# Performance work log

Hardware: AMD Instinct MI355X
Metric: run time of the kernel (lower is better)

The kernel has to match this reference:

```python
import jax, jax.numpy as jnp
import numpy as np

# CrossAttention (DFFNet): 1x1 convs produce q,k from depth and v from rgb;
# full dense attention over hw spatial tokens: softmax(q^T k) then v @ mask^T.

def setup_inputs() -> dict:
    key = jax.random.key(0)
    ks = jax.random.split(key, 8)
    B, C, H, W = 4, 256, 64, 64
    Cqk = C // 8  # ratio=8 -> 32
    s = 0.02
    return {
        "rgb":   jax.random.normal(ks[0], (B, C, H, W), jnp.float32),
        "depth": jax.random.normal(ks[1], (B, C, H, W), jnp.float32),
        "Wq": jax.random.normal(ks[2], (Cqk, C), jnp.float32) * s,
        "bq": jax.random.normal(ks[3], (Cqk,), jnp.float32) * s,
        "Wk": jax.random.normal(ks[4], (Cqk, C), jnp.float32) * s,
        "bk": jax.random.normal(ks[5], (Cqk,), jnp.float32) * s,
        "Wv": jax.random.normal(ks[6], (C, C), jnp.float32) * s,
        "bv": jax.random.normal(ks[7], (C,), jnp.float32) * s,
    }


def reference(rgb, depth, Wq, bq, Wk, bk, Wv, bv):
    B, C, H, W = rgb.shape
    hw = H * W
    d = depth.reshape(B, C, hw)   # [B, C, hw]
    r = rgb.reshape(B, C, hw)     # [B, C, hw]
    # 1x1 convs == channel-mixing linear maps
    q = jnp.einsum('oc,bcn->bon', Wq, d) + bq[None, :, None]  # [B, Cqk, hw]
    k = jnp.einsum('oc,bcn->bon', Wk, d) + bk[None, :, None]  # [B, Cqk, hw]
    v = jnp.einsum('oc,bcn->bon', Wv, r) + bv[None, :, None]  # [B, C, hw]
    # scores: q^T k -> [B, hw, hw], softmax over last dim
    scores = jnp.einsum('bcn,bcm->bnm', q, k)
    mask = jax.nn.softmax(scores, axis=-1)
    # feat = v @ mask^T  -> [B, C, hw]
    feat = jnp.einsum('bcm,bnm->bcn', v, mask)
    return feat.reshape(B, C, H, W)
```

## Files before the change

### kernel.cpp

```cpp
#include <hip/hip_runtime.h>
#include <stdint.h>

#define L2E 1.44269504088896340736f

typedef _Float16 half8 __attribute__((ext_vector_type(8)));
typedef float floatx4 __attribute__((ext_vector_type(4)));

static __device__ __forceinline__ unsigned short f32_to_f16u(float f) {
  union { _Float16 h; unsigned short s; } cv; cv.h = (_Float16)f; return cv.s;
}

typedef __attribute__((address_space(3))) unsigned int as3_uint;
typedef __attribute__((address_space(1))) const unsigned int as1_cuint;

static __device__ __forceinline__ void async16(const void* g, void* l) {
  __builtin_amdgcn_global_load_lds((as1_cuint*)g, (as3_uint*)l, 16, 0, 0);
}

__global__ __launch_bounds__(256) void proj_kernel(
    const float* __restrict__ rgb,
    const float* __restrict__ depth,
    const float* __restrict__ Wq, const float* __restrict__ bq,
    const float* __restrict__ Wk, const float* __restrict__ bk,
    const float* __restrict__ Wv, const float* __restrict__ bv,
    unsigned short* __restrict__ qT,
    unsigned short* __restrict__ kT,
    unsigned short* __restrict__ v)
{
  __shared__ __align__(16) unsigned short sW[64 * 256];

  const int n0 = blockIdx.x * 64;
  const int b  = blockIdx.y;
  const int z  = blockIdx.z;
  const int t  = threadIdx.x;
  const int w  = t >> 6;
  const int lane = t & 63;
  const int l15 = lane & 15;
  const int q4  = lane >> 4;

  const float* X = (z == 0) ? depth : rgb;
  const float* xb = X + (size_t)b * 256 * 4096;
  const int n_row = n0 + 16 * w + l15;

  half8 a8[8];
#pragma unroll
  for (int ks = 0; ks < 8; ks++) {
#pragma unroll
    for (int j = 0; j < 8; j++) {
      int c = ks * 32 + q4 * 8 + j;
      a8[ks][j] = (_Float16)xb[(size_t)c * 4096 + n_row];
    }
  }

  const int nq = (z == 0) ? 1 : 2;
  for (int qd = 0; qd < nq; qd++) {
    const int colbase = (z == 0) ? 0 : (z - 1) * 128 + qd * 64;
    __syncthreads();

#pragma unroll
    for (int it = 0; it < 8; it++) {
      int L = it * 256 + t;
      int og = L >> 5;
      int phys = L & 31;
      int ci = phys ^ (og & 7);
      const float* wr;
      if (z == 0) wr = (og < 32) ? (Wq + (size_t)og * 256) : (Wk + (size_t)(og - 32) * 256);
      else        wr = Wv + (size_t)(colbase + og) * 256;
      float4 w0 = *(const float4*)(wr + ci * 8);
      float4 w1 = *(const float4*)(wr + ci * 8 + 4);
      half8 h;
      h[0] = (_Float16)w0.x; h[1] = (_Float16)w0.y; h[2] = (_Float16)w0.z; h[3] = (_Float16)w0.w;
      h[4] = (_Float16)w1.x; h[5] = (_Float16)w1.y; h[6] = (_Float16)w1.z; h[7] = (_Float16)w1.w;
      *(half8*)&sW[(size_t)L * 8] = h;
    }

    float bias[4];
#pragma unroll
    for (int ct = 0; ct < 4; ct++) {
      int og = ct * 16 + l15;
      if (z == 0) bias[ct] = (og < 32) ? bq[og] : bk[og - 32];
      else        bias[ct] = bv[colbase + og];
    }
    __syncthreads();

    floatx4 acc[4];
#pragma unroll
    for (int i = 0; i < 4; i++) acc[i] = (floatx4){0.f, 0.f, 0.f, 0.f};

#pragma unroll
    for (int ks = 0; ks < 8; ks++) {
      const int ci = ks * 4 + q4;
#pragma unroll
      for (int ct = 0; ct < 4; ct++) {
        int og = ct * 16 + l15;
        half8 bf = *(const half8*)&sW[og * 256 + ((ci ^ (og & 7)) * 8)];
        acc[ct] = __builtin_amdgcn_mfma_f32_16x16x32_f16(a8[ks], bf, acc[ct], 0, 0, 0);
      }
    }

    __syncthreads();

    if (z == 0) {
#pragma unroll
      for (int ct = 0; ct < 4; ct++) {
        int og = ct * 16 + l15;
#pragma unroll
        for (int r = 0; r < 4; r++) {
          int n = n0 + 16 * w + q4 * 4 + r;
          unsigned short hv = f32_to_f16u(acc[ct][r] + bias[ct]);
          if (og < 32) qT[((size_t)b * 4096 + n) * 32 + og] = hv;
          else         kT[((size_t)b * 4096 + n) * 32 + (og - 32)] = hv;
        }
      }
    } else {
      unsigned short* tile = sW;
#pragma unroll
      for (int ct = 0; ct < 4; ct++) {
#pragma unroll
        for (int r = 0; r < 4; r++) {
          int co_l = ct * 16 + l15;
          int nl = 16 * w + q4 * 4 + r;
          tile[co_l * 72 + nl] = f32_to_f16u(acc[ct][r] + bias[ct]);
        }
      }
      __syncthreads();
#pragma unroll
      for (int it = 0; it < 2; it++) {
        int co_l = it * 32 + (t >> 3);
        int ch = t & 7;
        int4 val = *(const int4*)&tile[co_l * 72 + ch * 8];
        *(int4*)&v[((size_t)b * 256 + colbase + co_l) * 4096 + n0 + ch * 8] = val;
      }
    }
  }
}

static __device__ __forceinline__ void stage_v(
    const unsigned short* __restrict__ vB, unsigned char* sbase,
    int m0, int t, int w)
{
#pragma unroll
  for (int j = 0; j < 4; j++) {
    int lin = j * 256 + t;
    int c = lin >> 2;
    int p = lin & 3;
    int lc = p ^ ((c >> 1) & 3);
    async16(&vB[(size_t)c * 4096 + m0 + lc * 8], sbase + j * 4096 + w * 1024);
  }
}

__global__ __launch_bounds__(256, 4) void attn_kernel(
    const unsigned short* __restrict__ qT,
    const unsigned short* __restrict__ kT,
    const unsigned short* __restrict__ v,
    unsigned short* __restrict__ Op,
    float* __restrict__ lW)
{
  __shared__ __align__(16) unsigned char smem[37888];
  unsigned short* sP = (unsigned short*)(smem + 32768);

  const int n0 = blockIdx.x * 64;
  const int b  = blockIdx.y;
  const int chunk = blockIdx.z;
  const int t  = threadIdx.x;
  const int w  = t >> 6;
  const int lane = t & 63;
  const int l15 = lane & 15;
  const int q4  = lane >> 4;

  half8 aq = *(const half8*)(qT + ((size_t)b * 4096 + n0 + 16 * w + l15) * 32 + q4 * 8);

  const unsigned short* vB = v + (size_t)b * 256 * 4096;
  const unsigned short* kL = kT + (size_t)b * 4096 * 32 + (size_t)l15 * 32 + q4 * 8;
  unsigned short* sPw = sP + w * 640;

  float lsum[4] = {0.f, 0.f, 0.f, 0.f};
  floatx4 acc[16];
#pragma unroll
  for (int ct = 0; ct < 16; ct++) acc[ct] = (floatx4){0.f, 0.f, 0.f, 0.f};
  const floatx4 zf = (floatx4){0.f, 0.f, 0.f, 0.f};

  const int mbase = chunk * 1024;

  stage_v(vB, smem, mbase, t, w);
  half8 kc0 = *(const half8*)(kL + (size_t)mbase * 32);
  half8 kc1 = *(const half8*)(kL + (size_t)(mbase + 16) * 32);

  int bufoff = 0;
  for (int it = 0; it < 32; ++it) {
    const int m0 = mbase + it * 32;
    half8 kn0 = kc0, kn1 = kc1;
    if (it < 31) {
      stage_v(vB, smem + (bufoff ^ 16384), m0 + 32, t, w);
      kn0 = *(const half8*)(kL + (size_t)(m0 + 32) * 32);
      kn1 = *(const half8*)(kL + (size_t)(m0 + 48) * 32);
      asm volatile("s_waitcnt vmcnt(6)" ::: "memory");
    } else {
      asm volatile("s_waitcnt vmcnt(0)" ::: "memory");
    }

    floatx4 s0 = __builtin_amdgcn_mfma_f32_16x16x32_f16(aq, kc0, zf, 0, 0, 0);
    floatx4 s1 = __builtin_amdgcn_mfma_f32_16x16x32_f16(aq, kc1, zf, 0, 0, 0);

    float p0[4], p1[4];
#pragma unroll
    for (int r = 0; r < 4; r++) {
      p0[r] = exp2f(s0[r] * L2E);
      p1[r] = exp2f(s1[r] * L2E);
      lsum[r] += p0[r] + p1[r];
    }
#pragma unroll
    for (int r = 0; r < 4; r++) {
      int row = q4 * 4 + r;
      sPw[row * 40 + l15]      = f32_to_f16u(p0[r]);
      sPw[row * 40 + 16 + l15] = f32_to_f16u(p1[r]);
    }
    asm volatile("s_waitcnt lgkmcnt(0)" ::: "memory");

    __builtin_amdgcn_s_barrier();
    asm volatile("s_waitcnt lgkmcnt(0)" ::: "memory");

    half8 ap[4];
#pragma unroll
    for (int nt = 0; nt < 4; nt++)
      ap[nt] = *(const half8*)&sP[nt * 640 + l15 * 40 + q4 * 8];

    const unsigned short* sVb = (const unsigned short*)(smem + bufoff);
#pragma unroll
    for (int ct = 0; ct < 4; ct++) {
      int co = w * 64 + ct * 16 + l15;
      half8 bv8 = *(const half8*)&sVb[co * 32 + ((q4 ^ ((co >> 1) & 3)) * 8)];
#pragma unroll
      for (int nt = 0; nt < 4; nt++)
        acc[ct * 4 + nt] = __builtin_amdgcn_mfma_f32_16x16x32_f16(ap[nt], bv8, acc[ct * 4 + nt], 0, 0, 0);
    }
    asm volatile("s_waitcnt lgkmcnt(0)" ::: "memory");
    __builtin_amdgcn_s_barrier();

    kc0 = kn0; kc1 = kn1;
    bufoff ^= 16384;
  }

#pragma unroll
  for (int off = 1; off < 16; off <<= 1) {
#pragma unroll
    for (int r = 0; r < 4; r++) lsum[r] += __shfl_xor(lsum[r], off);
  }
  if (l15 == 0) {
#pragma unroll
    for (int r = 0; r < 4; r++)
      lW[((size_t)chunk * 4 + b) * 4096 + n0 + 16 * w + q4 * 4 + r] = lsum[r];
  }

  unsigned short* sO = (unsigned short*)smem;
#pragma unroll
  for (int pass = 0; pass < 2; pass++) {
    __syncthreads();
    if ((w >> 1) == pass) {
#pragma unroll
      for (int ct = 0; ct < 4; ct++) {
        int co_l = (w & 1) * 64 + ct * 16 + l15;
#pragma unroll
        for (int nt = 0; nt < 4; nt++) {
#pragma unroll
          for (int r = 0; r < 4; r++) {
            int nl = nt * 16 + q4 * 4 + r;
            sO[co_l * 72 + nl] = f32_to_f16u(acc[ct * 4 + nt][r]);
          }
        }
      }
    }
    __syncthreads();
#pragma unroll
    for (int s = 0; s < 4; s++) {
      int co_l = s * 32 + (t >> 3);
      int ch = t & 7;
      int4 val = *(const int4*)&sO[co_l * 72 + ch * 8];
      *(int4*)&Op[(((size_t)chunk * 4 + b) * 256 + pass * 128 + co_l) * 4096 + n0 + ch * 8] = val;
    }
  }
}

__global__ __launch_bounds__(256) void combine_kernel(
    const unsigned short* __restrict__ Op,
    const float* __restrict__ lW,
    float* __restrict__ out)
{
  const int t = threadIdx.x;
  const int b = blockIdx.y;
  const size_t n8 = (size_t)blockIdx.x * 2048 + (size_t)t * 8;
  const int co0 = blockIdx.z * 8;

  float sum[8] = {0.f, 0.f, 0.f, 0.f, 0.f, 0.f, 0.f, 0.f};
#pragma unroll
  for (int ch = 0; ch < 4; ch++) {
    const float* lp = lW + ((size_t)ch * 4 + b) * 4096 + n8;
    float4 a0 = *(const float4*)lp;
    float4 a1 = *(const float4*)(lp + 4);
    sum[0] += a0.x; sum[1] += a0.y; sum[2] += a0.z; sum[3] += a0.w;
    sum[4] += a1.x; sum[5] += a1.y; sum[6] += a1.z; sum[7] += a1.w;
  }
  float rl[8];
#pragma unroll
  for (int i = 0; i < 8; i++) rl[i] = 1.0f / sum[i];

#pragma unroll
  for (int cc = 0; cc < 8; cc++) {
    int co = co0 + cc;
    float o[8] = {0.f, 0.f, 0.f, 0.f, 0.f, 0.f, 0.f, 0.f};
#pragma unroll
    for (int ch = 0; ch < 4; ch++) {
      half8 hv = *(const half8*)&Op[(((size_t)ch * 4 + b) * 256 + co) * 4096 + n8];
#pragma unroll
      for (int i = 0; i < 8; i++) o[i] += (float)hv[i];
    }
    float* op = out + ((size_t)b * 256 + co) * 4096 + n8;
    float4 r0, r1;
    r0.x = o[0] * rl[0]; r0.y = o[1] * rl[1]; r0.z = o[2] * rl[2]; r0.w = o[3] * rl[3];
    r1.x = o[4] * rl[4]; r1.y = o[5] * rl[5]; r1.z = o[6] * rl[6]; r1.w = o[7] * rl[7];
    *(float4*)op = r0;
    *(float4*)(op + 4) = r1;
  }
}

extern "C" void kernel_launch(void* const* d_in, const int* in_sizes, int n_in,
                              void* d_out, int out_size, void* d_ws, size_t ws_size,
                              hipStream_t stream) {
  const float* rgb   = (const float*)d_in[0];
  const float* depth = (const float*)d_in[1];
  const float* Wq    = (const float*)d_in[2];
  const float* bq    = (const float*)d_in[3];
  const float* Wk    = (const float*)d_in[4];
  const float* bk    = (const float*)d_in[5];
  const float* Wv    = (const float*)d_in[6];
  const float* bv    = (const float*)d_in[7];
  float* out = (float*)d_out;

  unsigned short* qT = (unsigned short*)d_ws;
  unsigned short* kT = qT + (size_t)4 * 4096 * 32;
  unsigned short* vW = kT + (size_t)4 * 4096 * 32;
  unsigned short* Op = vW + (size_t)4 * 256 * 4096;
  float* lW = (float*)(Op + (size_t)4 * 4 * 256 * 4096);

  dim3 pg(64, 4, 3);
  proj_kernel<<<pg, 256, 0, stream>>>(rgb, depth, Wq, bq, Wk, bk, Wv, bv, qT, kT, vW);
  dim3 ag(64, 4, 4);
  attn_kernel<<<ag, 256, 0, stream>>>(qT, kT, vW, Op, lW);
  dim3 cg(2, 4, 32);
  combine_kernel<<<cg, 256, 0, stream>>>(Op, lW, out);
}
```

Before: 163.5 us.

## Load V fragments directly into registers and double-buffer P to drop a barrier

Replaces the async global-to-LDS staging of V with direct per-lane register loads of the V fragments each wave needs, prefetched one iteration ahead. The P tile in shared memory is double-buffered by iteration parity, which removes the second barrier per iteration and shrinks shared memory from about 37KB to 18KB. The exp2f call is replaced with a raw v_exp_f32 instruction. Register pressure rises from the extra prefetched V fragments, and the launch bound's min-blocks hint drops from 4 to 3. Direct global loads of V are strided rows of 16 bytes, which may coalesce worse than the LDS staging did.

```diff
diff --git a/kernel.cpp b/kernel.cpp
--- a/kernel.cpp
+++ b/kernel.cpp
@@ -10,11 +10,10 @@
   union { _Float16 h; unsigned short s; } cv; cv.h = (_Float16)f; return cv.s;
 }
 
-typedef __attribute__((address_space(3))) unsigned int as3_uint;
-typedef __attribute__((address_space(1))) const unsigned int as1_cuint;
-
-static __device__ __forceinline__ void async16(const void* g, void* l) {
-  __builtin_amdgcn_global_load_lds((as1_cuint*)g, (as3_uint*)l, 16, 0, 0);
+static __device__ __forceinline__ float fast_exp2(float x) {
+  float r;
+  asm("v_exp_f32 %0, %1" : "=v"(r) : "v"(x));
+  return r;
 }
 
 __global__ __launch_bounds__(256) void proj_kernel(
@@ -135,29 +134,15 @@
   }
 }
 
-static __device__ __forceinline__ void stage_v(
-    const unsigned short* __restrict__ vB, unsigned char* sbase,
-    int m0, int t, int w)
-{
-#pragma unroll
-  for (int j = 0; j < 4; j++) {
-    int lin = j * 256 + t;
-    int c = lin >> 2;
-    int p = lin & 3;
-    int lc = p ^ ((c >> 1) & 3);
-    async16(&vB[(size_t)c * 4096 + m0 + lc * 8], sbase + j * 4096 + w * 1024);
-  }
-}
-
-__global__ __launch_bounds__(256, 4) void attn_kernel(
+__global__ __launch_bounds__(256, 3) void attn_kernel(
     const unsigned short* __restrict__ qT,
     const unsigned short* __restrict__ kT,
     const unsigned short* __restrict__ v,
     unsigned short* __restrict__ Op,
     float* __restrict__ lW)
 {
-  __shared__ __align__(16) unsigned char smem[37888];
-  unsigned short* sP = (unsigned short*)(smem + 32768);
+  __shared__ __align__(16) unsigned char smem[18432];
+  unsigned short* sP = (unsigned short*)smem;
 
   const int n0 = blockIdx.x * 64;
   const int b  = blockIdx.y;
@@ -170,9 +155,8 @@
 
   half8 aq = *(const half8*)(qT + ((size_t)b * 4096 + n0 + 16 * w + l15) * 32 + q4 * 8);
 
-  const unsigned short* vB = v + (size_t)b * 256 * 4096;
   const unsigned short* kL = kT + (size_t)b * 4096 * 32 + (size_t)l15 * 32 + q4 * 8;
-  unsigned short* sPw = sP + w * 640;
+  const unsigned short* vL = v + ((size_t)b * 256 + w * 64 + l15) * 4096 + q4 * 8;
 
   float lsum[4] = {0.f, 0.f, 0.f, 0.f};
   floatx4 acc[16];
@@ -182,21 +166,26 @@
 
   const int mbase = chunk * 1024;
 
-  stage_v(vB, smem, mbase, t, w);
   half8 kc0 = *(const half8*)(kL + (size_t)mbase * 32);
   half8 kc1 = *(const half8*)(kL + (size_t)(mbase + 16) * 32);
-
-  int bufoff = 0;
+  half8 vc0 = *(const half8*)(vL + mbase);
+  half8 vc1 = *(const half8*)(vL + 65536 + mbase);
+  half8 vc2 = *(const half8*)(vL + 131072 + mbase);
+  half8 vc3 = *(const half8*)(vL + 196608 + mbase);
+
+  unsigned short* sPw = sP + w * 640;
+
   for (int it = 0; it < 32; ++it) {
     const int m0 = mbase + it * 32;
-    half8 kn0 = kc0, kn1 = kc1;
+    const int bufo = (it & 1) * 2560;
+    half8 kn0 = kc0, kn1 = kc1, vn0 = vc0, vn1 = vc1, vn2 = vc2, vn3 = vc3;
     if (it < 31) {
-      stage_v(vB, smem + (bufoff ^ 16384), m0 + 32, t, w);
       kn0 = *(const half8*)(kL + (size_t)(m0 + 32) * 32);
       kn1 = *(const half8*)(kL + (size_t)(m0 + 48) * 32);
-      asm volatile("s_waitcnt vmcnt(6)" ::: "memory");
-    } else {
-      asm volatile("s_waitcnt vmcnt(0)" ::: "memory");
+      vn0 = *(const half8*)(vL + m0 + 32);
+      vn1 = *(const half8*)(vL + 65536 + m0 + 32);
+      vn2 = *(const half8*)(vL + 131072 + m0 + 32);
+      vn3 = *(const half8*)(vL + 196608 + m0 + 32);
     }
 
     floatx4 s0 = __builtin_amdgcn_mfma_f32_16x16x32_f16(aq, kc0, zf, 0, 0, 0);
@@ -205,40 +194,34 @@
     float p0[4], p1[4];
 #pragma unroll
     for (int r = 0; r < 4; r++) {
-      p0[r] = exp2f(s0[r] * L2E);
-      p1[r] = exp2f(s1[r] * L2E);
+      p0[r] = fast_exp2(s0[r] * L2E);
+      p1[r] = fast_exp2(s1[r] * L2E);
       lsum[r] += p0[r] + p1[r];
     }
 #pragma unroll
     for (int r = 0; r < 4; r++) {
       int row = q4 * 4 + r;
-      sPw[row * 40 + l15]      = f32_to_f16u(p0[r]);
-      sPw[row * 40 + 16 + l15] = f32_to_f16u(p1[r]);
+      sPw[bufo + row * 40 + l15]      = f32_to_f16u(p0[r]);
+      sPw[bufo + row * 40 + 16 + l15] = f32_to_f16u(p1[r]);
     }
     asm volatile("s_waitcnt lgkmcnt(0)" ::: "memory");
-
     __builtin_amdgcn_s_barrier();
-    asm volatile("s_waitcnt lgkmcnt(0)" ::: "memory");
+    asm volatile("" ::: "memory");
 
     half8 ap[4];
 #pragma unroll
     for (int nt = 0; nt < 4; nt++)
-      ap[nt] = *(const half8*)&sP[nt * 640 + l15 * 40 + q4 * 8];
-
-    const unsigned short* sVb = (const unsigned short*)(smem + bufoff);
+      ap[nt] = *(const half8*)&sP[bufo + nt * 640 + l15 * 40 + q4 * 8];
+
 #pragma unroll
     for (int ct = 0; ct < 4; ct++) {
-      int co = w * 64 + ct * 16 + l15;
-      half8 bv8 = *(const half8*)&sVb[co * 32 + ((q4 ^ ((co >> 1) & 3)) * 8)];
+      half8 bv8 = (ct == 0) ? vc0 : (ct == 1) ? vc1 : (ct == 2) ? vc2 : vc3;
 #pragma unroll
       for (int nt = 0; nt < 4; nt++)
         acc[ct * 4 + nt] = __builtin_amdgcn_mfma_f32_16x16x32_f16(ap[nt], bv8, acc[ct * 4 + nt], 0, 0, 0);
     }
-    asm volatile("s_waitcnt lgkmcnt(0)" ::: "memory");
-    __builtin_amdgcn_s_barrier();
-
-    kc0 = kn0; kc1 = kn1;
-    bufoff ^= 16384;
+
+    kc0 = kn0; kc1 = kn1; vc0 = vn0; vc1 = vn1; vc2 = vn2; vc3 = vn3;
   }
 
 #pragma unroll
```

Measured after the change: 180.8 us. 10.6% more time.
